# Optimization experiments

Measured on AMD Instinct MI355X. Metric: run time of the kernel, lower is better.

The kernel has to match this reference:

```python
import jax, jax.numpy as jnp
import numpy as np

D_MODEL = 1024
NHEAD = 16
HEAD_DIM = D_MODEL // NHEAD
B, S = 4, 2048


def setup_inputs() -> dict:
    key = jax.random.key(0)
    ks = jax.random.split(key, 10)
    scale = 1.0 / np.sqrt(D_MODEL)
    inp = {
        "x": jax.random.normal(ks[0], (B, S, D_MODEL), dtype=jnp.float32),
        "y": jax.random.normal(ks[1], (B, S, D_MODEL), dtype=jnp.float32),
        "wq": jax.random.normal(ks[2], (D_MODEL, D_MODEL), dtype=jnp.float32) * scale,
        "bq": jnp.zeros((D_MODEL,), dtype=jnp.float32),
        "wk": jax.random.normal(ks[3], (D_MODEL, D_MODEL), dtype=jnp.float32) * scale,
        "bk": jnp.zeros((D_MODEL,), dtype=jnp.float32),
        "wv": jax.random.normal(ks[4], (D_MODEL, D_MODEL), dtype=jnp.float32) * scale,
        "bv": jnp.zeros((D_MODEL,), dtype=jnp.float32),
        "wo": jax.random.normal(ks[5], (D_MODEL, D_MODEL), dtype=jnp.float32) * scale,
        "bo": jnp.zeros((D_MODEL,), dtype=jnp.float32),
    }
    return inp


def reference(x, y, wq, bq, wk, bk, wv, bv, wo, bo):
    # Linear projections (torch nn.Linear: x @ W.T + b; here weights stored as [in, out])
    q = x @ wq + bq  # [B, S, D]
    k = y @ wk + bk
    v = y @ wv + bv
    # split heads -> [B, H, S, Dh]
    def heads(t):
        return t.reshape(B, S, NHEAD, HEAD_DIM).transpose(0, 2, 1, 3)
    q, k, v = heads(q), heads(k), heads(v)
    scores = jnp.einsum("bhqd,bhkd->bhqk", q, k) / jnp.sqrt(jnp.float32(HEAD_DIM))
    attn = jax.nn.softmax(scores, axis=-1)  # dropout = identity in eval mode
    out = jnp.einsum("bhqk,bhkd->bhqd", attn, v)
    out = out.transpose(0, 2, 1, 3).reshape(B, S, D_MODEL)
    return out @ wo + bo
```

## Files before the change

### kernel.cpp

```cpp
#include <hip/hip_runtime.h>
#include <stdint.h>

#define D_MODEL 1024
#define NHEAD 16
#define HEAD_DIM 64
#define BATCH 4
#define SEQ 2048
#define ROWS (BATCH*SEQ)

typedef __attribute__((ext_vector_type(8))) short short8;
typedef __attribute__((ext_vector_type(4))) float f32x4;
typedef __attribute__((ext_vector_type(2))) unsigned int u32x2;
typedef unsigned short u16;
typedef unsigned int u32;

#define QSCALE 0.18033688011112042f

__device__ __forceinline__ u16 f2b(float f) {
  union { float f; uint32_t u; } in; in.f = f;
  uint32_t u = in.u;
  return (u16)((u + 0x7FFFu + ((u >> 16) & 1u)) >> 16);
}

__device__ __forceinline__ void async_lds16(const void* g, void* l) {
  __builtin_amdgcn_global_load_lds(
      (const __attribute__((address_space(1))) uint32_t*)g,
      (__attribute__((address_space(3))) uint32_t*)l,
      16, 0, 0);
}

__device__ __forceinline__ u32 pack_bf16(float lo, float hi) {
  union { float f; uint32_t u; } a, b; a.f = lo; b.f = hi;
  return __builtin_amdgcn_perm(b.u + 0x8000u, a.u + 0x8000u, 0x07060302u);
}

__global__ void __launch_bounds__(256) cvt_kernel(const float* __restrict__ x,
                                                  const float* __restrict__ y,
                                                  u16* __restrict__ xb,
                                                  u16* __restrict__ yb) {
  const float* in = blockIdx.y ? y : x;
  u16* out = blockIdx.y ? yb : xb;
  int i = blockIdx.x * 256 + threadIdx.x;
  float4 v = ((const float4*)in)[i];
  ushort4 o;
  o.x = f2b(v.x); o.y = f2b(v.y); o.z = f2b(v.z); o.w = f2b(v.w);
  ((ushort4*)out)[i] = o;
}

__global__ void __launch_bounds__(256) wtrans_kernel(const float* __restrict__ wq,
                                                     const float* __restrict__ wk,
                                                     const float* __restrict__ wv,
                                                     const float* __restrict__ wo,
                                                     u16* __restrict__ wtbase) {
  __shared__ u16 tile[64 * 65];
  int z = blockIdx.z;
  const float* w = (z == 0) ? wq : (z == 1 ? wk : (z == 2 ? wv : wo));
  u16* wt = wtbase + (size_t)z * D_MODEL * D_MODEL;
  int t = threadIdx.x;
  int c = t & 63, rb = t >> 6;
  int k0 = blockIdx.x * 64, n0 = blockIdx.y * 64;
#pragma unroll
  for (int i = 0; i < 16; ++i) {
    int r = rb + i * 4;
    tile[c * 65 + r] = f2b(w[(size_t)(k0 + r) * D_MODEL + n0 + c]);
  }
  __syncthreads();
#pragma unroll
  for (int i = 0; i < 16; ++i) {
    int r = rb + i * 4;
    wt[(size_t)(n0 + r) * D_MODEL + k0 + c] = tile[r * 65 + c];
  }
}

template <int MODE>
__device__ __forceinline__ void gemm_bt_core(const u16* __restrict__ A,
                                             const u16* __restrict__ Bt,
                                             const float* __restrict__ bias,
                                             void* __restrict__ Cout, float scale,
                                             int m0, int n0) {
  constexpr int K = 1024, N = 1024;
  __shared__ u16 As[128 * 32];
  __shared__ u16 Bs[128 * 32];
  int tid = threadIdx.x;
  int wave = tid >> 6, lane = tid & 63;
  int quad = lane >> 4, l16 = lane & 15;
  int wm = wave & 1, wn = wave >> 1;

  f32x4 acc[4][4];
#pragma unroll
  for (int mi = 0; mi < 4; ++mi)
#pragma unroll
    for (int ni = 0; ni < 4; ++ni) acc[mi][ni] = f32x4{0.f, 0.f, 0.f, 0.f};

  int srow = lane >> 2;
  int scol = (lane & 3) * 16;

  for (int k0 = 0; k0 < K; k0 += 32) {
#pragma unroll
    for (int i = 0; i < 2; ++i) {
      int c = wave * 2 + i;
      const char* ga = (const char*)(A + (size_t)(m0 + c * 16 + srow) * K + k0) + scol;
      async_lds16(ga, (char*)As + c * 1024);
      const char* gb = (const char*)(Bt + (size_t)(n0 + c * 16 + srow) * K + k0) + scol;
      async_lds16(gb, (char*)Bs + c * 1024);
    }
    __syncthreads();

    short8 af[4], bf[4];
#pragma unroll
    for (int mi = 0; mi < 4; ++mi)
      af[mi] = *(const short8*)(As + (wm * 64 + mi * 16 + l16) * 32 + quad * 8);
#pragma unroll
    for (int ni = 0; ni < 4; ++ni)
      bf[ni] = *(const short8*)(Bs + (wn * 64 + ni * 16 + l16) * 32 + quad * 8);
#pragma unroll
    for (int mi = 0; mi < 4; ++mi)
#pragma unroll
      for (int ni = 0; ni < 4; ++ni)
        acc[mi][ni] = __builtin_amdgcn_mfma_f32_16x16x32_bf16(af[mi], bf[ni], acc[mi][ni], 0, 0, 0);
    __syncthreads();
  }

  if (MODE == 2) {
#pragma unroll
    for (int ni = 0; ni < 4; ++ni) {
      int col = n0 + wn * 64 + ni * 16 + l16;
      int bb = col >> 11, ss = col & 2047;
      size_t sbase = (size_t)(ss & ~63) + 4 * l16 + ni;
#pragma unroll
      for (int mi = 0; mi < 4; ++mi) {
        int row0 = m0 + wm * 64 + mi * 16 + quad * 4;
#pragma unroll
        for (int r = 0; r < 4; ++r) {
          int dcol = row0 + r;
          float vv = acc[mi][ni][r] + bias[dcol];
          int hh = dcol >> 6, dd = dcol & 63;
          size_t vtrow = ((size_t)bb * 16 + hh) * 64 + dd;
          ((u16*)Cout)[vtrow * 2048 + sbase] = f2b(vv);
        }
      }
    }
  } else {
#pragma unroll
    for (int ni = 0; ni < 4; ++ni) {
      int col = n0 + wn * 64 + ni * 16 + l16;
      float bv = bias[col];
#pragma unroll
      for (int mi = 0; mi < 4; ++mi) {
        int row = m0 + wm * 64 + mi * 16 + quad * 4;
#pragma unroll
        for (int r = 0; r < 4; ++r) {
          float vv = (acc[mi][ni][r] + bv) * scale;
          if (MODE == 1)
            ((float*)Cout)[(size_t)(row + r) * N + col] = vv;
          else
            ((u16*)Cout)[(size_t)(row + r) * N + col] = f2b(vv);
        }
      }
    }
  }
}

__global__ void __launch_bounds__(256) gemm_qkv_kernel(
    const u16* __restrict__ xb, const u16* __restrict__ yb,
    const u16* __restrict__ wqT, const u16* __restrict__ wkT, const u16* __restrict__ wvT,
    const float* __restrict__ bq, const float* __restrict__ bk, const float* __restrict__ bv,
    u16* __restrict__ q, u16* __restrict__ k, u16* __restrict__ vt) {
  int bx = blockIdx.x, z = blockIdx.y;
  if (z == 0) {
    gemm_bt_core<0>(xb, wqT, bq, q, QSCALE, (bx >> 3) * 128, (bx & 7) * 128);
  } else if (z == 1) {
    gemm_bt_core<0>(yb, wkT, bk, k, 1.0f, (bx >> 3) * 128, (bx & 7) * 128);
  } else {
    gemm_bt_core<2>(wvT, yb, bv, vt, 1.0f, (bx & 7) * 128, (bx >> 3) * 128);
  }
}

__global__ void __launch_bounds__(256) gemm_o_kernel(const u16* __restrict__ ao,
                                                     const u16* __restrict__ woT,
                                                     const float* __restrict__ bo,
                                                     float* __restrict__ out) {
  gemm_bt_core<1>(ao, woT, bo, out, 1.0f, blockIdx.y * 128, blockIdx.x * 128);
}

__global__ void __launch_bounds__(256, 4) attn_kernel(const u16* __restrict__ Q,
                                                      const u16* __restrict__ Kp,
                                                      const u16* __restrict__ Vt,
                                                      u16* __restrict__ Outp) {
  __shared__ u16 Ks[2][64 * 64];
  __shared__ u16 Vts[2][64 * 64];
  __shared__ u16 Ps[4][32 * 64];

  int tid = threadIdx.x, wave = tid >> 6, lane = tid & 63;
  int quad = lane >> 4, l16 = lane & 15;
  int bh = blockIdx.x;
  int b = bh >> 4, h = bh & 15;
  int q0 = blockIdx.y * 128 + wave * 32;
  size_t gbase = (size_t)b * SEQ * D_MODEL;
  const u16* kbase = Kp + gbase + (size_t)h * HEAD_DIM;
  const u16* vbase = Vt + (size_t)bh * HEAD_DIM * SEQ;
  const u16* qrow = Q + gbase + (size_t)q0 * D_MODEL + (size_t)h * HEAD_DIM;

  short8 aq[2][2];
#pragma unroll
  for (int rs = 0; rs < 2; ++rs)
#pragma unroll
    for (int dc = 0; dc < 2; ++dc)
      aq[rs][dc] = *(const short8*)(qrow + (size_t)(rs * 16 + l16) * D_MODEL + dc * 32 + quad * 8);

  f32x4 Oacc[2][4];
  float lpart[2][4];
#pragma unroll
  for (int rs = 0; rs < 2; ++rs)
#pragma unroll
    for (int ni = 0; ni < 4; ++ni) Oacc[rs][ni] = f32x4{0.f, 0.f, 0.f, 0.f};
#pragma unroll
  for (int rs = 0; rs < 2; ++rs)
#pragma unroll
    for (int r = 0; r < 4; ++r) lpart[rs][r] = 0.f;

  size_t koff[2], voff[2];
  int dstoff[2];
#pragma unroll
  for (int i = 0; i < 2; ++i) {
    int c = i * 256 + tid;
    int krow = c >> 3, kgp = c & 7;
    koff[i] = (size_t)krow * D_MODEL + (size_t)((kgp ^ (krow & 7)) * 8);
    voff[i] = (size_t)krow * SEQ + (size_t)((kgp ^ (krow & 7)) * 8);
    dstoff[i] = i * 4096 + wave * 1024;
  }

#pragma unroll
  for (int i = 0; i < 2; ++i) {
    async_lds16(kbase + koff[i], (char*)Ks[0] + dstoff[i]);
    async_lds16(vbase + voff[i], (char*)Vts[0] + dstoff[i]);
  }

  constexpr int NT = SEQ / 64;
  for (int t = 0; t < NT; ++t) {
    int cur = t & 1;
    __syncthreads();
    if (t + 1 < NT) {
      size_t kvoff = (size_t)(t + 1) * 64;
#pragma unroll
      for (int i = 0; i < 2; ++i) {
        async_lds16(kbase + kvoff * D_MODEL + koff[i], (char*)Ks[cur ^ 1] + dstoff[i]);
        async_lds16(vbase + kvoff + voff[i], (char*)Vts[cur ^ 1] + dstoff[i]);
      }
    }

    const u16* Kc = Ks[cur];
    const u16* Vc = Vts[cur];
    u16* Pw = Ps[wave];
    int x = l16 & 7;

    short8 kf[4][2];
#pragma unroll
    for (int sub = 0; sub < 4; ++sub) {
      const u16* kr = Kc + (sub * 16 + l16) * 64;
      kf[sub][0] = *(const short8*)(kr + ((quad ^ x) << 3));
      kf[sub][1] = *(const short8*)(kr + (((4 + quad) ^ x) << 3));
    }

#pragma unroll
    for (int rs = 0; rs < 2; ++rs) {
      f32x4 S[4];
#pragma unroll
      for (int sub = 0; sub < 4; ++sub) {
        f32x4 s = f32x4{0.f, 0.f, 0.f, 0.f};
        s = __builtin_amdgcn_mfma_f32_16x16x32_bf16(aq[rs][0], kf[sub][0], s, 0, 0, 0);
        s = __builtin_amdgcn_mfma_f32_16x16x32_bf16(aq[rs][1], kf[sub][1], s, 0, 0, 0);
        S[sub] = s;
      }
#pragma unroll
      for (int r = 0; r < 4; ++r) {
        float p0 = __builtin_amdgcn_exp2f(S[0][r]);
        float p1 = __builtin_amdgcn_exp2f(S[1][r]);
        float p2 = __builtin_amdgcn_exp2f(S[2][r]);
        float p3 = __builtin_amdgcn_exp2f(S[3][r]);
        lpart[rs][r] += (p0 + p1) + (p2 + p3);
        u32 lo = pack_bf16(p0, p1);
        u32 hi = pack_bf16(p2, p3);
        int row = rs * 16 + quad * 4 + r;
        int off = row * 64 + (((l16 >> 1) ^ (row & 7)) << 3) + ((l16 & 1) << 2);
        *(u32x2*)(Pw + off) = u32x2{lo, hi};
      }
    }

#pragma unroll
    for (int kc = 0; kc < 2; ++kc) {
      short8 pa[2];
#pragma unroll
      for (int rs = 0; rs < 2; ++rs) {
        int prow = rs * 16 + l16;
        pa[rs] = *(const short8*)(Pw + prow * 64 + ((((kc << 2) + quad) ^ x) << 3));
      }
#pragma unroll
      for (int ni = 0; ni < 4; ++ni) {
        int d = ni * 16 + l16;
        short8 bv = *(const short8*)(Vc + d * 64 + ((((kc << 2) + quad) ^ (l16 & 7)) << 3));
        Oacc[0][ni] = __builtin_amdgcn_mfma_f32_16x16x32_bf16(pa[0], bv, Oacc[0][ni], 0, 0, 0);
        Oacc[1][ni] = __builtin_amdgcn_mfma_f32_16x16x32_bf16(pa[1], bv, Oacc[1][ni], 0, 0, 0);
      }
    }
  }

#pragma unroll
  for (int rs = 0; rs < 2; ++rs)
#pragma unroll
    for (int r = 0; r < 4; ++r) {
      float l = lpart[rs][r];
      l += __shfl_xor(l, 1);
      l += __shfl_xor(l, 2);
      l += __shfl_xor(l, 4);
      l += __shfl_xor(l, 8);
      float inv = 1.0f / l;
      size_t orow = gbase + (size_t)(q0 + rs * 16 + quad * 4 + r) * D_MODEL + (size_t)h * HEAD_DIM;
#pragma unroll
      for (int ni = 0; ni < 4; ++ni)
        Outp[orow + ni * 16 + l16] = f2b(Oacc[rs][ni][r] * inv);
    }
}

extern "C" void kernel_launch(void* const* d_in, const int* in_sizes, int n_in,
                              void* d_out, int out_size, void* d_ws, size_t ws_size,
                              hipStream_t stream) {
  const float* x  = (const float*)d_in[0];
  const float* y  = (const float*)d_in[1];
  const float* wq = (const float*)d_in[2];
  const float* bq = (const float*)d_in[3];
  const float* wk = (const float*)d_in[4];
  const float* bk = (const float*)d_in[5];
  const float* wv = (const float*)d_in[6];
  const float* bv = (const float*)d_in[7];
  const float* wo = (const float*)d_in[8];
  const float* bo = (const float*)d_in[9];
  float* out = (float*)d_out;

  char* ws = (char*)d_ws;
  const size_t SZ_ACT = (size_t)ROWS * D_MODEL * 2;
  const size_t SZ_W   = (size_t)D_MODEL * D_MODEL * 2;
  u16* xb  = (u16*)(ws);
  u16* yb  = (u16*)(ws + SZ_ACT);
  u16* wT  = (u16*)(ws + 2 * SZ_ACT);
  u16* wqT = wT;
  u16* wkT = (u16*)(ws + 2 * SZ_ACT + SZ_W);
  u16* wvT = (u16*)(ws + 2 * SZ_ACT + 2 * SZ_W);
  u16* woT = (u16*)(ws + 2 * SZ_ACT + 3 * SZ_W);
  u16* qb  = (u16*)(ws + 2 * SZ_ACT + 4 * SZ_W);
  u16* kb  = (u16*)(ws + 3 * SZ_ACT + 4 * SZ_W);
  u16* vt  = (u16*)(ws + 4 * SZ_ACT + 4 * SZ_W);
  u16* ao  = (u16*)(ws + 5 * SZ_ACT + 4 * SZ_W);

  cvt_kernel<<<dim3(8192, 2), 256, 0, stream>>>(x, y, xb, yb);
  wtrans_kernel<<<dim3(16, 16, 4), 256, 0, stream>>>(wq, wk, wv, wo, wT);
  gemm_qkv_kernel<<<dim3(512, 3), 256, 0, stream>>>(xb, yb, wqT, wkT, wvT, bq, bk, bv, qb, kb, vt);
  attn_kernel<<<dim3(64, 16), 256, 0, stream>>>(qb, kb, vt, ao);
  gemm_o_kernel<<<dim3(8, 64), 256, 0, stream>>>(ao, woT, bo, out);
}
```

Before: 352.2 us.

## Deepen GEMM K-step, vectorize epilogue stores, drop attention double buffering

The GEMM core now stages two 32-wide K slices per barrier (K step 64), which halves the number of sync points. For the non-V modes it swaps MFMA operand order so each lane holds four contiguous output columns, allowing vectorized bf16/f32 stores with float4 bias loads. The V-transpose path packs four outputs into one 8-byte store, and both GEMM kernels get a minimum-occupancy launch bound. Separately, the attention kernel drops K/V double buffering in favour of a single buffer with load-then-sync. This saves LDS but exposes global load latency on every tile.

```diff
diff --git a/kernel.cpp b/kernel.cpp
--- a/kernel.cpp
+++ b/kernel.cpp
@@ -79,8 +79,9 @@
                                              void* __restrict__ Cout, float scale,
                                              int m0, int n0) {
   constexpr int K = 1024, N = 1024;
-  __shared__ u16 As[128 * 32];
-  __shared__ u16 Bs[128 * 32];
+  constexpr bool SWAP = (MODE != 2);
+  __shared__ u16 As[2][128 * 32];
+  __shared__ u16 Bs[2][128 * 32];
   int tid = threadIdx.x;
   int wave = tid >> 6, lane = tid & 63;
   int quad = lane >> 4, l16 = lane & 15;
@@ -88,80 +89,90 @@
 
   f32x4 acc[4][4];
 #pragma unroll
-  for (int mi = 0; mi < 4; ++mi)
-#pragma unroll
-    for (int ni = 0; ni < 4; ++ni) acc[mi][ni] = f32x4{0.f, 0.f, 0.f, 0.f};
+  for (int p = 0; p < 4; ++p)
+#pragma unroll
+    for (int q = 0; q < 4; ++q) acc[p][q] = f32x4{0.f, 0.f, 0.f, 0.f};
 
   int srow = lane >> 2;
   int scol = (lane & 3) * 16;
 
-  for (int k0 = 0; k0 < K; k0 += 32) {
-#pragma unroll
-    for (int i = 0; i < 2; ++i) {
-      int c = wave * 2 + i;
-      const char* ga = (const char*)(A + (size_t)(m0 + c * 16 + srow) * K + k0) + scol;
-      async_lds16(ga, (char*)As + c * 1024);
-      const char* gb = (const char*)(Bt + (size_t)(n0 + c * 16 + srow) * K + k0) + scol;
-      async_lds16(gb, (char*)Bs + c * 1024);
+  for (int k0 = 0; k0 < K; k0 += 64) {
+#pragma unroll
+    for (int kh = 0; kh < 2; ++kh) {
+#pragma unroll
+      for (int i = 0; i < 2; ++i) {
+        int c = wave * 2 + i;
+        const char* ga = (const char*)(A + (size_t)(m0 + c * 16 + srow) * K + k0 + kh * 32) + scol;
+        async_lds16(ga, (char*)As[kh] + c * 1024);
+        const char* gb = (const char*)(Bt + (size_t)(n0 + c * 16 + srow) * K + k0 + kh * 32) + scol;
+        async_lds16(gb, (char*)Bs[kh] + c * 1024);
+      }
     }
     __syncthreads();
 
-    short8 af[4], bf[4];
-#pragma unroll
-    for (int mi = 0; mi < 4; ++mi)
-      af[mi] = *(const short8*)(As + (wm * 64 + mi * 16 + l16) * 32 + quad * 8);
-#pragma unroll
-    for (int ni = 0; ni < 4; ++ni)
-      bf[ni] = *(const short8*)(Bs + (wn * 64 + ni * 16 + l16) * 32 + quad * 8);
-#pragma unroll
-    for (int mi = 0; mi < 4; ++mi)
-#pragma unroll
-      for (int ni = 0; ni < 4; ++ni)
-        acc[mi][ni] = __builtin_amdgcn_mfma_f32_16x16x32_bf16(af[mi], bf[ni], acc[mi][ni], 0, 0, 0);
+#pragma unroll
+    for (int kh = 0; kh < 2; ++kh) {
+      short8 fa[4], fb[4];
+#pragma unroll
+      for (int p = 0; p < 4; ++p)
+        fa[p] = SWAP
+          ? *(const short8*)(Bs[kh] + (wn * 64 + p * 16 + l16) * 32 + quad * 8)
+          : *(const short8*)(As[kh] + (wm * 64 + p * 16 + l16) * 32 + quad * 8);
+#pragma unroll
+      for (int q = 0; q < 4; ++q)
+        fb[q] = SWAP
+          ? *(const short8*)(As[kh] + (wm * 64 + q * 16 + l16) * 32 + quad * 8)
+          : *(const short8*)(Bs[kh] + (wn * 64 + q * 16 + l16) * 32 + quad * 8);
+#pragma unroll
+      for (int p = 0; p < 4; ++p)
+#pragma unroll
+        for (int q = 0; q < 4; ++q)
+          acc[p][q] = __builtin_amdgcn_mfma_f32_16x16x32_bf16(fa[p], fb[q], acc[p][q], 0, 0, 0);
+    }
     __syncthreads();
   }
 
   if (MODE == 2) {
-#pragma unroll
-    for (int ni = 0; ni < 4; ++ni) {
-      int col = n0 + wn * 64 + ni * 16 + l16;
-      int bb = col >> 11, ss = col & 2047;
-      size_t sbase = (size_t)(ss & ~63) + 4 * l16 + ni;
-#pragma unroll
-      for (int mi = 0; mi < 4; ++mi) {
-        int row0 = m0 + wm * 64 + mi * 16 + quad * 4;
-#pragma unroll
-        for (int r = 0; r < 4; ++r) {
-          int dcol = row0 + r;
-          float vv = acc[mi][ni][r] + bias[dcol];
-          int hh = dcol >> 6, dd = dcol & 63;
-          size_t vtrow = ((size_t)bb * 16 + hh) * 64 + dd;
-          ((u16*)Cout)[vtrow * 2048 + sbase] = f2b(vv);
+    int sblk = n0 + wn * 64;
+    int bb = sblk >> 11;
+    int ssb = sblk & 2047;
+#pragma unroll
+    for (int p = 0; p < 4; ++p) {
+      int dbase = m0 + wm * 64 + p * 16 + quad * 4;
+      float4 b4 = *(const float4*)(bias + dbase);
+#pragma unroll
+      for (int r = 0; r < 4; ++r) {
+        int d = dbase + r;
+        float bv = ((const float*)&b4)[r];
+        u32 lo = pack_bf16(acc[p][0][r] + bv, acc[p][1][r] + bv);
+        u32 hi = pack_bf16(acc[p][2][r] + bv, acc[p][3][r] + bv);
+        size_t vtrow = ((size_t)bb * 16 + (d >> 6)) * 64 + (d & 63);
+        *(u32x2*)((u16*)Cout + vtrow * 2048 + ssb + 4 * l16) = u32x2{lo, hi};
+      }
+    }
+  } else {
+#pragma unroll
+    for (int p = 0; p < 4; ++p) {
+      int nbase = n0 + wn * 64 + p * 16 + quad * 4;
+      float4 b4 = *(const float4*)(bias + nbase);
+#pragma unroll
+      for (int q = 0; q < 4; ++q) {
+        size_t mrow = (size_t)(m0 + wm * 64 + q * 16 + l16);
+        float v0 = (acc[p][q][0] + b4.x) * scale;
+        float v1 = (acc[p][q][1] + b4.y) * scale;
+        float v2 = (acc[p][q][2] + b4.z) * scale;
+        float v3 = (acc[p][q][3] + b4.w) * scale;
+        if (MODE == 1) {
+          *(f32x4*)((float*)Cout + mrow * N + nbase) = f32x4{v0, v1, v2, v3};
+        } else {
+          *(u32x2*)((u16*)Cout + mrow * N + nbase) = u32x2{pack_bf16(v0, v1), pack_bf16(v2, v3)};
         }
       }
     }
-  } else {
-#pragma unroll
-    for (int ni = 0; ni < 4; ++ni) {
-      int col = n0 + wn * 64 + ni * 16 + l16;
-      float bv = bias[col];
-#pragma unroll
-      for (int mi = 0; mi < 4; ++mi) {
-        int row = m0 + wm * 64 + mi * 16 + quad * 4;
-#pragma unroll
-        for (int r = 0; r < 4; ++r) {
-          float vv = (acc[mi][ni][r] + bv) * scale;
-          if (MODE == 1)
-            ((float*)Cout)[(size_t)(row + r) * N + col] = vv;
-          else
-            ((u16*)Cout)[(size_t)(row + r) * N + col] = f2b(vv);
-        }
-      }
-    }
-  }
-}
-
-__global__ void __launch_bounds__(256) gemm_qkv_kernel(
+  }
+}
+
+__global__ void __launch_bounds__(256, 4) gemm_qkv_kernel(
     const u16* __restrict__ xb, const u16* __restrict__ yb,
     const u16* __restrict__ wqT, const u16* __restrict__ wkT, const u16* __restrict__ wvT,
     const float* __restrict__ bq, const float* __restrict__ bk, const float* __restrict__ bv,
@@ -176,10 +187,10 @@
   }
 }
 
-__global__ void __launch_bounds__(256) gemm_o_kernel(const u16* __restrict__ ao,
-                                                     const u16* __restrict__ woT,
-                                                     const float* __restrict__ bo,
-                                                     float* __restrict__ out) {
+__global__ void __launch_bounds__(256, 4) gemm_o_kernel(const u16* __restrict__ ao,
+                                                        const u16* __restrict__ woT,
+                                                        const float* __restrict__ bo,
+                                                        float* __restrict__ out) {
   gemm_bt_core<1>(ao, woT, bo, out, 1.0f, blockIdx.y * 128, blockIdx.x * 128);
 }
 
@@ -187,8 +198,8 @@
                                                       const u16* __restrict__ Kp,
                                                       const u16* __restrict__ Vt,
                                                       u16* __restrict__ Outp) {
-  __shared__ u16 Ks[2][64 * 64];
-  __shared__ u16 Vts[2][64 * 64];
+  __shared__ u16 Ks[64 * 64];
+  __shared__ u16 Vts[64 * 64];
   __shared__ u16 Ps[4][32 * 64];
 
   int tid = threadIdx.x, wave = tid >> 6, lane = tid & 63;
@@ -230,34 +241,22 @@
     dstoff[i] = i * 4096 + wave * 1024;
   }
 
-#pragma unroll
-  for (int i = 0; i < 2; ++i) {
-    async_lds16(kbase + koff[i], (char*)Ks[0] + dstoff[i]);
-    async_lds16(vbase + voff[i], (char*)Vts[0] + dstoff[i]);
-  }
-
-  constexpr int NT = SEQ / 64;
-  for (int t = 0; t < NT; ++t) {
-    int cur = t & 1;
+  for (int kv0 = 0; kv0 < SEQ; kv0 += 64) {
     __syncthreads();
-    if (t + 1 < NT) {
-      size_t kvoff = (size_t)(t + 1) * 64;
-#pragma unroll
-      for (int i = 0; i < 2; ++i) {
-        async_lds16(kbase + kvoff * D_MODEL + koff[i], (char*)Ks[cur ^ 1] + dstoff[i]);
-        async_lds16(vbase + kvoff + voff[i], (char*)Vts[cur ^ 1] + dstoff[i]);
-      }
-    }
-
-    const u16* Kc = Ks[cur];
-    const u16* Vc = Vts[cur];
+#pragma unroll
+    for (int i = 0; i < 2; ++i) {
+      async_lds16(kbase + (size_t)kv0 * D_MODEL + koff[i], (char*)Ks + dstoff[i]);
+      async_lds16(vbase + (size_t)kv0 + voff[i], (char*)Vts + dstoff[i]);
+    }
+    __syncthreads();
+
     u16* Pw = Ps[wave];
     int x = l16 & 7;
 
     short8 kf[4][2];
 #pragma unroll
     for (int sub = 0; sub < 4; ++sub) {
-      const u16* kr = Kc + (sub * 16 + l16) * 64;
+      const u16* kr = Ks + (sub * 16 + l16) * 64;
       kf[sub][0] = *(const short8*)(kr + ((quad ^ x) << 3));
       kf[sub][1] = *(const short8*)(kr + (((4 + quad) ^ x) << 3));
     }
@@ -298,7 +297,7 @@
 #pragma unroll
       for (int ni = 0; ni < 4; ++ni) {
         int d = ni * 16 + l16;
-        short8 bv = *(const short8*)(Vc + d * 64 + ((((kc << 2) + quad) ^ (l16 & 7)) << 3));
+        short8 bv = *(const short8*)(Vts + d * 64 + ((((kc << 2) + quad) ^ (l16 & 7)) << 3));
         Oacc[0][ni] = __builtin_amdgcn_mfma_f32_16x16x32_bf16(pa[0], bv, Oacc[0][ni], 0, 0, 0);
         Oacc[1][ni] = __builtin_amdgcn_mfma_f32_16x16x32_bf16(pa[1], bv, Oacc[1][ni], 0, 0, 0);
       }
```

Result: faster. 329.8 us (-6.4%).
